# Performance work log

Measured on AMD Instinct MI355X. Metric: run time of the kernel, lower is better.

The kernel has to match this reference:

```python
import jax, jax.numpy as jnp
import numpy as np
from jax.ops import segment_sum, segment_max

N_M = 100000   # muon nodes
N_J = 100000   # jet nodes
E   = 1600000  # edges per relation (~avg degree 16)
D   = 64       # input feature dim
H   = 64       # hidden_channels
C   = 2        # num_classes

def setup_inputs():
    key = jax.random.key(0)
    ks = jax.random.split(key, 16)
    g = lambda k, shape, fan: jax.random.normal(k, shape, jnp.float32) / np.sqrt(fan).astype(np.float32)
    return {
        "x_muons": jax.random.normal(ks[0], (N_M, D), jnp.float32),
        "x_jets":  jax.random.normal(ks[1], (N_J, D), jnp.float32),
        "ei_mm": jax.random.randint(ks[2], (2, E), 0, N_M, jnp.int32),
        "ei_mj": jnp.stack([jax.random.randint(ks[3], (E,), 0, N_M, jnp.int32),
                            jax.random.randint(ks[4], (E,), 0, N_J, jnp.int32)]),
        "ei_jj": jax.random.randint(ks[5], (2, E), 0, N_J, jnp.int32),
        "gat_w_src": g(ks[6], (D, H), D),
        "gat_w_dst": g(ks[7], (D, H), D),
        "gat_att_src": g(ks[8], (H,), H),
        "gat_att_dst": g(ks[9], (H,), H),
        "gat_bias": jnp.zeros((H,), jnp.float32),
        "sage_w_l": g(ks[10], (D, H), D),
        "sage_w_r": g(ks[11], (D, H), D),
        "sage_bias": jnp.zeros((H,), jnp.float32),
        "gcn_w": g(ks[12], (D, H), D),
        "gcn_bias": jnp.zeros((H,), jnp.float32),
        "lin_w": g(ks[13], (H, C), H),
        "lin_b": jnp.zeros((C,), jnp.float32),
    }

def _add_self_loops(ei, n):
    loop = jnp.arange(n, dtype=ei.dtype)
    return jnp.concatenate([ei[0], loop]), jnp.concatenate([ei[1], loop])

def _gat(x, ei, w_src, w_dst, att_src, att_dst, bias):
    # PyG GATConv, heads=1, add_self_loops=True, negative_slope=0.2
    n = x.shape[0]
    src, dst = _add_self_loops(ei, n)
    hs = x @ w_src                      # [n, H] source-side messages
    hd = x @ w_dst                      # dst-side (attention only)
    a = jax.nn.leaky_relu((hs @ att_src)[src] + (hd @ att_dst)[dst], 0.2)
    m = segment_max(a, dst, num_segments=n)      # per-dst softmax (stable)
    ea = jnp.exp(a - m[dst])
    z = segment_sum(ea, dst, num_segments=n)
    alpha = ea / z[dst]                 # self loop guarantees z > 0
    return segment_sum(alpha[:, None] * hs[src], dst, num_segments=n) + bias

def _sage(x_src, x_dst, ei, w_l, w_r, bias):
    # PyG SAGEConv: mean aggregation, root weight, no self loops
    n = x_dst.shape[0]
    src, dst = ei[0], ei[1]
    agg = segment_sum(x_src[src], dst, num_segments=n)
    cnt = segment_sum(jnp.ones_like(dst, jnp.float32), dst, num_segments=n)
    mean = agg / jnp.maximum(cnt, 1.0)[:, None]
    return mean @ w_l + x_dst @ w_r + bias

def _gcn(x, ei, w, bias):
    # PyG GCNConv: symmetric gcn_norm on A + I
    n = x.shape[0]
    src, dst = _add_self_loops(ei, n)
    xw = x @ w
    deg = segment_sum(jnp.ones_like(dst, jnp.float32), dst, num_segments=n)
    dis = deg ** -0.5                   # deg >= 1 due to self loops
    norm = dis[src] * dis[dst]
    return segment_sum(norm[:, None] * xw[src], dst, num_segments=n) + bias

def reference(x_muons, x_jets, ei_mm, ei_mj, ei_jj,
              gat_w_src, gat_w_dst, gat_att_src, gat_att_dst, gat_bias,
              sage_w_l, sage_w_r, sage_bias, gcn_w, gcn_bias, lin_w, lin_b):
    # Original forward returns inside the layer loop -> exactly one HeteroConv layer runs.
    muons = _gat(x_muons, ei_mm, gat_w_src, gat_w_dst, gat_att_src, gat_att_dst, gat_bias)
    jets = (_sage(x_muons, x_jets, ei_mj, sage_w_l, sage_w_r, sage_bias)
            + _gcn(x_jets, ei_jj, gcn_w, gcn_bias))   # HeteroConv aggr='sum' on dst type 'jets'
    muons = jax.nn.relu(muons)
    jets = jax.nn.relu(jets)
    out = jnp.concatenate([muons, jets], axis=0)       # [N_M + N_J, H]
    return jax.nn.sigmoid(out @ lin_w + lin_b)
```

## Files before the change

kernel.cpp:

```cpp
#include <hip/hip_runtime.h>
#include <math.h>

#define N_M 100000
#define N_J 100000
#define NE  1600000
#define NTOT (3*N_M)
#define ETOT (3*NE)
#define NB_SCAN 293
#define DD  64
#define HH  64

#define NBIN 586
#define BIN_SHIFT 9
#define G1 640
#define EPB ((ETOT + G1 - 1) / G1)

__device__ __forceinline__ float lrelu(float a){ return a > 0.f ? a : 0.2f*a; }
__device__ __forceinline__ float wmax(float v){
    #pragma unroll
    for (int o = 32; o; o >>= 1) v = fmaxf(v, __shfl_xor(v, o));
    return v;
}
__device__ __forceinline__ float wsum(float v){
    #pragma unroll
    for (int o = 32; o; o >>= 1) v += __shfl_xor(v, o);
    return v;
}
__device__ __forceinline__ float sigm(float x){ return 1.f/(1.f + expf(-x)); }

__device__ __forceinline__ unsigned short f2bf(float f){
    unsigned u = __float_as_uint(f);
    u += 0x7FFFu + ((u >> 16) & 1u);
    return (unsigned short)(u >> 16);
}
__device__ __forceinline__ float bf2f(unsigned short h){
    return __uint_as_float((unsigned)h << 16);
}


__global__ void k_vdst(const float* __restrict__ w_dst, const float* __restrict__ att_dst,
                       float* __restrict__ v_dst){
    int d = threadIdx.x;
    float s = 0.f;
    for (int h = 0; h < HH; ++h) s += w_dst[d*HH + h] * att_dst[h];
    v_dst[d] = s;
}

__global__ __launch_bounds__(256) void k_muon_prep(
    const float* __restrict__ x, const float* __restrict__ w_src,
    const float* __restrict__ att_src, const float* __restrict__ v_dst,
    unsigned short* __restrict__ hs_b, float* __restrict__ as_, float* __restrict__ ad_)
{
    __shared__ float lw[DD*HH];
    __shared__ float latt[HH];
    __shared__ float lvd[DD];
    int tid = threadIdx.x;
    for (int i = tid; i < DD*HH; i += 256) lw[i] = w_src[i];
    if (tid < HH) latt[tid] = att_src[tid];
    if (tid < DD) lvd[tid] = v_dst[tid];
    __syncthreads();
    int row = blockIdx.x*64 + (tid >> 2);
    int q = tid & 3;
    if (row >= N_M) return;
    const float4* x4 = (const float4*)(x + (size_t)row*DD);
    float acc[16];
    #pragma unroll
    for (int f = 0; f < 16; ++f) acc[f] = 0.f;
    float adp = 0.f;
    for (int kk = 0; kk < 16; ++kk){
        float4 xv = x4[kk];
        adp += xv.x*lvd[4*kk] + xv.y*lvd[4*kk+1] + xv.z*lvd[4*kk+2] + xv.w*lvd[4*kk+3];
        float xs[4] = {xv.x, xv.y, xv.z, xv.w};
        #pragma unroll
        for (int j = 0; j < 4; ++j){
            const float* wp = lw + (4*kk + j)*HH + (q << 4);
            float xk = xs[j];
            #pragma unroll
            for (int f = 0; f < 16; ++f) acc[f] = fmaf(xk, wp[f], acc[f]);
        }
    }
    float asp = 0.f;
    #pragma unroll
    for (int f = 0; f < 16; ++f) asp += acc[f] * latt[(q<<4) + f];
    asp += __shfl_xor(asp, 1);
    asp += __shfl_xor(asp, 2);
    unsigned short* hp = hs_b + (size_t)row*HH + (q << 4);
    #pragma unroll
    for (int j = 0; j < 4; ++j)
        ((ushort4*)hp)[j] = make_ushort4(f2bf(acc[4*j]), f2bf(acc[4*j+1]),
                                         f2bf(acc[4*j+2]), f2bf(acc[4*j+3]));
    if (q == 0){ as_[row] = asp; ad_[row] = adp; }
}

__global__ __launch_bounds__(256) void k_gcn_xw(
    const float* __restrict__ x, const float* __restrict__ w, unsigned short* __restrict__ xw_b)
{
    __shared__ float lw[DD*HH];
    int tid = threadIdx.x;
    for (int i = tid; i < DD*HH; i += 256) lw[i] = w[i];
    __syncthreads();
    int row = blockIdx.x*64 + (tid >> 2);
    int q = tid & 3;
    if (row >= N_J) return;
    const float4* x4 = (const float4*)(x + (size_t)row*DD);
    float acc[16];
    #pragma unroll
    for (int f = 0; f < 16; ++f) acc[f] = 0.f;
    for (int kk = 0; kk < 16; ++kk){
        float4 xv = x4[kk];
        float xs[4] = {xv.x, xv.y, xv.z, xv.w};
        #pragma unroll
        for (int j = 0; j < 4; ++j){
            const float* wp = lw + (4*kk + j)*HH + (q << 4);
            float xk = xs[j];
            #pragma unroll
            for (int f = 0; f < 16; ++f) acc[f] = fmaf(xk, wp[f], acc[f]);
        }
    }
    unsigned short* hp = xw_b + (size_t)row*HH + (q << 4);
    #pragma unroll
    for (int j = 0; j < 4; ++j)
        ((ushort4*)hp)[j] = make_ushort4(f2bf(acc[4*j]), f2bf(acc[4*j+1]),
                                         f2bf(acc[4*j+2]), f2bf(acc[4*j+3]));
}

__global__ __launch_bounds__(256) void k_xr(
    const float* __restrict__ x, const float* __restrict__ w_r,
    const float* __restrict__ sb, const float* __restrict__ gb, float* __restrict__ xr)
{
    __shared__ float lw[DD*HH];
    __shared__ float lb[HH];
    int tid = threadIdx.x;
    for (int i = tid; i < DD*HH; i += 256) lw[i] = w_r[i];
    if (tid < HH) lb[tid] = sb[tid] + gb[tid];
    __syncthreads();
    int row = blockIdx.x*64 + (tid >> 2);
    int q = tid & 3;
    if (row >= N_J) return;
    const float4* x4 = (const float4*)(x + (size_t)row*DD);
    float acc[16];
    #pragma unroll
    for (int f = 0; f < 16; ++f) acc[f] = 0.f;
    for (int kk = 0; kk < 16; ++kk){
        float4 xv = x4[kk];
        float xs[4] = {xv.x, xv.y, xv.z, xv.w};
        #pragma unroll
        for (int j = 0; j < 4; ++j){
            const float* wp = lw + (4*kk + j)*HH + (q << 4);
            float xk = xs[j];
            #pragma unroll
            for (int f = 0; f < 16; ++f) acc[f] = fmaf(xk, wp[f], acc[f]);
        }
    }
    float* hp = xr + (size_t)row*HH + (q << 4);
    #pragma unroll
    for (int j = 0; j < 4; ++j){
        int f0 = (q << 4) + 4*j;
        ((float4*)hp)[j] = make_float4(acc[4*j]   + lb[f0],
                                       acc[4*j+1] + lb[f0+1],
                                       acc[4*j+2] + lb[f0+2],
                                       acc[4*j+3] + lb[f0+3]);
    }
}

__global__ void k_xm(const float* __restrict__ x, unsigned short* __restrict__ xb){
    int i = blockIdx.x*256 + threadIdx.x;
    if (i >= N_M*DD/4) return;
    float4 v = ((const float4*)x)[i];
    ((ushort4*)xb)[i] = make_ushort4(f2bf(v.x), f2bf(v.y), f2bf(v.z), f2bf(v.w));
}


__device__ __forceinline__ void edge_rd(int t, const int* ei_mm, const int* ei_mj,
                                        const int* ei_jj, const int** ei, int* r, int* e){
    if (t < NE){ *r = 0; *e = t; *ei = ei_mm; }
    else if (t < 2*NE){ *r = 1; *e = t - NE; *ei = ei_mj; }
    else { *r = 2; *e = t - 2*NE; *ei = ei_jj; }
}

__global__ __launch_bounds__(256) void k_bin0(
    const int* __restrict__ ei_mm, const int* __restrict__ ei_mj,
    const int* __restrict__ ei_jj, int* __restrict__ g_bincnt)
{
    __shared__ int bh[NBIN];
    int tid = threadIdx.x;
    for (int i = tid; i < NBIN; i += 256) bh[i] = 0;
    __syncthreads();
    int t0 = blockIdx.x * EPB;
    int t1 = min(t0 + EPB, ETOT);
    for (int t = t0 + tid; t < t1; t += 256){
        const int* ei; int r, e;
        edge_rd(t, ei_mm, ei_mj, ei_jj, &ei, &r, &e);
        int bucket = r*N_M + ei[NE + e];
        atomicAdd(&bh[bucket >> BIN_SHIFT], 1);
    }
    __syncthreads();
    for (int i = tid; i < NBIN; i += 256)
        if (bh[i]) atomicAdd(&g_bincnt[i], bh[i]);
}

__global__ void k_binscan(const int* __restrict__ g_bincnt, int* __restrict__ g_binoff,
                          int* __restrict__ g_bincur, int* __restrict__ offs)
{
    int l = threadIdx.x;
    int base = l * 10;
    int v[10]; int s = 0;
    #pragma unroll
    for (int k = 0; k < 10; ++k){
        int idx = base + k;
        v[k] = (idx < NBIN) ? g_bincnt[idx] : 0;
        s += v[k];
    }
    int inc = s;
    #pragma unroll
    for (int o = 1; o < 64; o <<= 1){
        int u = __shfl_up(inc, o);
        if (l >= o) inc += u;
    }
    int ex = inc - s;
    #pragma unroll
    for (int k = 0; k < 10; ++k){
        int idx = base + k;
        if (idx < NBIN){ g_binoff[idx] = ex; g_bincur[idx] = ex; ex += v[k]; }
    }
    if (l == 63) g_binoff[NBIN] = ex;
    if (l == 0)  offs[NTOT] = ETOT;
}

__global__ __launch_bounds__(256) void k_bin1(
    const int* __restrict__ ei_mm, const int* __restrict__ ei_mj,
    const int* __restrict__ ei_jj, int* __restrict__ g_bincur,
    unsigned* __restrict__ binned)
{
    __shared__ int bh[NBIN];
    __shared__ int cb[NBIN];
    int tid = threadIdx.x;
    for (int i = tid; i < NBIN; i += 256) bh[i] = 0;
    __syncthreads();
    int t0 = blockIdx.x * EPB;
    int t1 = min(t0 + EPB, ETOT);
    for (int t = t0 + tid; t < t1; t += 256){
        const int* ei; int r, e;
        edge_rd(t, ei_mm, ei_mj, ei_jj, &ei, &r, &e);
        int bucket = r*N_M + ei[NE + e];
        atomicAdd(&bh[bucket >> BIN_SHIFT], 1);
    }
    __syncthreads();
    for (int i = tid; i < NBIN; i += 256){
        int c = bh[i];
        cb[i] = c ? atomicAdd(&g_bincur[i], c) : 0;
        bh[i] = 0;
    }
    __syncthreads();
    for (int t = t0 + tid; t < t1; t += 256){
        const int* ei; int r, e;
        edge_rd(t, ei_mm, ei_mj, ei_jj, &ei, &r, &e);
        int s = ei[e];
        int bucket = r*N_M + ei[NE + e];
        int bin = bucket >> BIN_SHIFT;
        int lb  = bucket & 511;
        int pos = cb[bin] + atomicAdd(&bh[bin], 1);
        binned[pos] = ((unsigned)lb << 17) | (unsigned)s;
    }
}

__global__ __launch_bounds__(256) void k_build(
    const unsigned* __restrict__ binned, const int* __restrict__ g_binoff,
    int* __restrict__ offs, int* __restrict__ perm)
{
    __shared__ int lh[512];
    __shared__ int lcur[512];
    __shared__ int ls[256];
    int b = blockIdx.x, tid = threadIdx.x;
    int e0 = g_binoff[b], e1 = g_binoff[b+1];
    lh[tid] = 0; lh[tid + 256] = 0;
    __syncthreads();
    for (int e = e0 + tid; e < e1; e += 256)
        atomicAdd(&lh[binned[e] >> 17], 1);
    __syncthreads();
    int a0 = lh[2*tid], a1 = lh[2*tid + 1];
    int s = a0 + a1;
    ls[tid] = s; __syncthreads();
    for (int o = 1; o < 256; o <<= 1){
        int u = (tid >= o) ? ls[tid - o] : 0;
        __syncthreads();
        ls[tid] += u;
        __syncthreads();
    }
    int ex = ls[tid] - s;
    lcur[2*tid]     = ex;
    lcur[2*tid + 1] = ex + a0;
    int gb = b*512 + 2*tid;
    if (gb     < NTOT) offs[gb]     = e0 + ex;
    if (gb + 1 < NTOT) offs[gb + 1] = e0 + ex + a0;
    __syncthreads();
    for (int e = e0 + tid; e < e1; e += 256){
        unsigned p = binned[e];
        int pos = atomicAdd(&lcur[p >> 17], 1);
        perm[e0 + pos] = (int)(p & 0x1FFFFu);
    }
}


__global__ void k_hist(const int* __restrict__ ei_mm, const int* __restrict__ ei_mj,
                       const int* __restrict__ ei_jj, int* __restrict__ cnt){
    int t = blockIdx.x*256 + threadIdx.x;
    if (t >= ETOT) return;
    const int* ei; int r, e;
    edge_rd(t, ei_mm, ei_mj, ei_jj, &ei, &r, &e);
    atomicAdd(&cnt[r*N_M + ei[NE + e]], 1);
}

__global__ __launch_bounds__(256) void k_scan1(const int* __restrict__ cnt,
                                               int* __restrict__ offs, int* __restrict__ bsum){
    __shared__ int ls[256];
    int b = blockIdx.x, t = threadIdx.x;
    int base = b*1024 + t*4;
    int4 c = make_int4(0,0,0,0);
    if (base < NTOT) c = *(const int4*)(cnt + base);
    int s = c.x + c.y + c.z + c.w;
    ls[t] = s; __syncthreads();
    for (int o = 1; o < 256; o <<= 1){
        int a = (t >= o) ? ls[t - o] : 0;
        __syncthreads();
        ls[t] += a;
        __syncthreads();
    }
    int excl = ls[t] - s;
    if (t == 255) bsum[b] = ls[255];
    if (base < NTOT){
        offs[base]   = excl;
        offs[base+1] = excl + c.x;
        offs[base+2] = excl + c.x + c.y;
        offs[base+3] = excl + c.x + c.y + c.z;
    }
}

__global__ __launch_bounds__(512) void k_scan2(int* __restrict__ bsum){
    __shared__ int ls[512];
    int t = threadIdx.x;
    int v = (t < NB_SCAN) ? bsum[t] : 0;
    ls[t] = v; __syncthreads();
    for (int o = 1; o < 512; o <<= 1){
        int a = (t >= o) ? ls[t - o] : 0;
        __syncthreads();
        ls[t] += a;
        __syncthreads();
    }
    if (t < NB_SCAN) bsum[t] = ls[t] - v;
}

__global__ void k_scan3(int* __restrict__ offs, const int* __restrict__ bsum){
    int b = blockIdx.x, t = threadIdx.x;
    int base = b*1024 + t*4;
    if (base >= NTOT) return;
    int add = bsum[b];
    int4* p = (int4*)(offs + base);
    int4 v = *p;
    v.x += add; v.y += add; v.z += add; v.w += add;
    *p = v;
}

__global__ void k_fill(const int* __restrict__ ei_mm, const int* __restrict__ ei_mj,
                       const int* __restrict__ ei_jj, const int* __restrict__ offs,
                       int* __restrict__ cursor, int* __restrict__ perm){
    int t = blockIdx.x*256 + threadIdx.x;
    if (t >= ETOT) return;
    const int* ei; int r, e;
    edge_rd(t, ei_mm, ei_mj, ei_jj, &ei, &r, &e);
    int s = ei[e];
    int bkt = r*N_M + ei[NE + e];
    int pos = atomicAdd(&cursor[bkt], 1);
    perm[offs[bkt] + pos] = s;
}

__global__ void k_set_offs_top(int* __restrict__ offs){ offs[NTOT] = ETOT; }

__global__ void k_dis(const int* __restrict__ offs, float* __restrict__ dis){
    int j = blockIdx.x*256 + threadIdx.x;
    if (j >= N_J) return;
    int beg = offs[2*N_M + j];
    int end = (j == N_J-1) ? ETOT : offs[2*N_M + j + 1];
    dis[j] = rsqrtf((float)(end - beg + 1));
}


__global__ __launch_bounds__(512) void k_muon_gat_out(
    const int* __restrict__ offs, const int* __restrict__ perm,
    const float* __restrict__ as_, const float* __restrict__ ad_,
    const unsigned short* __restrict__ hs_b, const float* __restrict__ gat_bias,
    const float* __restrict__ lin_w, const float* __restrict__ lin_b,
    float* __restrict__ out)
{
    int wid = threadIdx.x >> 6;
    int l = threadIdx.x & 63;
    int d = blockIdx.x*8 + wid;
    if (d >= N_M) return;
    int p = l & 15, g = l >> 4;
    int beg = offs[d], end = offs[d+1];
    float ad_d = ad_[d];
    float a_self = lrelu(as_[d] + ad_d);
    float am = a_self;
    for (int base = beg; base < end; base += 64){
        int e = base + l;
        if (e < end) am = fmaxf(am, lrelu(as_[perm[e]] + ad_d));
    }
    float m = wmax(am);
    float eself = expf(a_self - m);
    float z = eself;
    float acc0 = 0.f, acc1 = 0.f, acc2 = 0.f, acc3 = 0.f;
    for (int base = beg; base < end; base += 64){
        int e = base + l;
        int sB = 0; float eaB = 0.f;
        if (e < end){
            sB = perm[e];
            eaB = expf(lrelu(as_[sB] + ad_d) - m);
        }
        z += wsum(eaB);
        int cc = min(64, end - base);
        int k = 0;
        for (; k + 16 <= cc; k += 16){
            #pragma unroll
            for (int qq = 0; qq < 4; ++qq){
                int idx = k + qq*4 + g;
                int s = __shfl(sB, idx);
                float w = __shfl(eaB, idx);
                ushort4 v = *(const ushort4*)(hs_b + (size_t)s*HH + 4*p);
                acc0 = fmaf(w, bf2f(v.x), acc0);
                acc1 = fmaf(w, bf2f(v.y), acc1);
                acc2 = fmaf(w, bf2f(v.z), acc2);
                acc3 = fmaf(w, bf2f(v.w), acc3);
            }
        }
        for (; k < cc; k += 4){
            int idx = k + g;
            int cl = min(idx, cc - 1);
            int s = __shfl(sB, cl);
            float w = __shfl(eaB, cl);
            if (idx >= cc) w = 0.f;
            ushort4 v = *(const ushort4*)(hs_b + (size_t)s*HH + 4*p);
            acc0 = fmaf(w, bf2f(v.x), acc0);
            acc1 = fmaf(w, bf2f(v.y), acc1);
            acc2 = fmaf(w, bf2f(v.z), acc2);
            acc3 = fmaf(w, bf2f(v.w), acc3);
        }
    }
    acc0 += __shfl_xor(acc0, 16); acc0 += __shfl_xor(acc0, 32);
    acc1 += __shfl_xor(acc1, 16); acc1 += __shfl_xor(acc1, 32);
    acc2 += __shfl_xor(acc2, 16); acc2 += __shfl_xor(acc2, 32);
    acc3 += __shfl_xor(acc3, 16); acc3 += __shfl_xor(acc3, 32);
    ushort4 hv = *(const ushort4*)(hs_b + (size_t)d*HH + 4*p);
    acc0 = fmaf(eself, bf2f(hv.x), acc0);
    acc1 = fmaf(eself, bf2f(hv.y), acc1);
    acc2 = fmaf(eself, bf2f(hv.z), acc2);
    acc3 = fmaf(eself, bf2f(hv.w), acc3);
    float rz = 1.f / z;
    float q0 = 0.f, q1 = 0.f;
    {
        float a[4] = {acc0, acc1, acc2, acc3};
        #pragma unroll
        for (int c = 0; c < 4; ++c){
            int f = 4*p + c;
            float val = fmaxf(a[c]*rz + gat_bias[f], 0.f);
            q0 = fmaf(val, lin_w[f*2 + 0], q0);
            q1 = fmaf(val, lin_w[f*2 + 1], q1);
        }
    }
    #pragma unroll
    for (int o = 1; o <= 8; o <<= 1){ q0 += __shfl_xor(q0, o); q1 += __shfl_xor(q1, o); }
    if (l == 0){
        size_t oo = (size_t)d*2;
        out[oo]   = sigm(q0 + lin_b[0]);
        out[oo+1] = sigm(q1 + lin_b[1]);
    }
}

__global__ __launch_bounds__(512) void k_jet_out(
    const unsigned short* __restrict__ xm_b, const unsigned short* __restrict__ xw_b,
    const float* __restrict__ xr, const float* __restrict__ dis,
    const int* __restrict__ offs, const int* __restrict__ perm,
    const float* __restrict__ w_l,
    const float* __restrict__ lin_w, const float* __restrict__ lin_b,
    float* __restrict__ out)
{
    __shared__ float lwl[DD*HH];
    int tid = threadIdx.x;
    for (int i = tid; i < DD*HH; i += 512) lwl[i] = w_l[i];
    __syncthreads();
    int wid = tid >> 6;
    int l = tid & 63;
    int j = blockIdx.x*8 + wid;
    if (j >= N_J) return;
    int p = l & 15, g = l >> 4;
    int beg = offs[N_M + j], end = offs[N_M + j + 1];
    float sa0 = 0.f, sa1 = 0.f, sa2 = 0.f, sa3 = 0.f;
    for (int base = beg; base < end; base += 64){
        int e = base + l;
        int sB = (e < end) ? perm[e] : 0;
        int cc = min(64, end - base);
        int k = 0;
        for (; k + 16 <= cc; k += 16){
            #pragma unroll
            for (int qq = 0; qq < 4; ++qq){
                int idx = k + qq*4 + g;
                int s = __shfl(sB, idx);
                ushort4 v = *(const ushort4*)(xm_b + (size_t)s*DD + 4*p);
                sa0 += bf2f(v.x); sa1 += bf2f(v.y); sa2 += bf2f(v.z); sa3 += bf2f(v.w);
            }
        }
        for (; k < cc; k += 4){
            int idx = k + g;
            int cl = min(idx, cc - 1);
            int s = __shfl(sB, cl);
            float w = (idx < cc) ? 1.f : 0.f;
            ushort4 v = *(const ushort4*)(xm_b + (size_t)s*DD + 4*p);
            sa0 = fmaf(w, bf2f(v.x), sa0);
            sa1 = fmaf(w, bf2f(v.y), sa1);
            sa2 = fmaf(w, bf2f(v.z), sa2);
            sa3 = fmaf(w, bf2f(v.w), sa3);
        }
    }
    sa0 += __shfl_xor(sa0, 16); sa0 += __shfl_xor(sa0, 32);
    sa1 += __shfl_xor(sa1, 16); sa1 += __shfl_xor(sa1, 32);
    sa2 += __shfl_xor(sa2, 16); sa2 += __shfl_xor(sa2, 32);
    sa3 += __shfl_xor(sa3, 16); sa3 += __shfl_xor(sa3, 32);
    float inv = (end > beg) ? 1.f/(float)(end - beg) : 1.f;
    float mean_a[4] = {sa0*inv, sa1*inv, sa2*inv, sa3*inv};
    int beg2 = offs[2*N_M + j];
    int end2 = (j == N_J-1) ? ETOT : offs[2*N_M + j + 1];
    float dj = dis[j];
    float gc0 = 0.f, gc1 = 0.f, gc2 = 0.f, gc3 = 0.f;
    for (int base = beg2; base < end2; base += 64){
        int e = base + l;
        int sB = 0; float nB = 0.f;
        if (e < end2){ sB = perm[e]; nB = dis[sB]*dj; }
        int cc = min(64, end2 - base);
        int k = 0;
        for (; k + 16 <= cc; k += 16){
            #pragma unroll
            for (int qq = 0; qq < 4; ++qq){
                int idx = k + qq*4 + g;
                int s = __shfl(sB, idx);
                float w = __shfl(nB, idx);
                ushort4 v = *(const ushort4*)(xw_b + (size_t)s*HH + 4*p);
                gc0 = fmaf(w, bf2f(v.x), gc0);
                gc1 = fmaf(w, bf2f(v.y), gc1);
                gc2 = fmaf(w, bf2f(v.z), gc2);
                gc3 = fmaf(w, bf2f(v.w), gc3);
            }
        }
        for (; k < cc; k += 4){
            int idx = k + g;
            int cl = min(idx, cc - 1);
            int s = __shfl(sB, cl);
            float w = __shfl(nB, cl);
            if (idx >= cc) w = 0.f;
            ushort4 v = *(const ushort4*)(xw_b + (size_t)s*HH + 4*p);
            gc0 = fmaf(w, bf2f(v.x), gc0);
            gc1 = fmaf(w, bf2f(v.y), gc1);
            gc2 = fmaf(w, bf2f(v.z), gc2);
            gc3 = fmaf(w, bf2f(v.w), gc3);
        }
    }
    gc0 += __shfl_xor(gc0, 16); gc0 += __shfl_xor(gc0, 32);
    gc1 += __shfl_xor(gc1, 16); gc1 += __shfl_xor(gc1, 32);
    gc2 += __shfl_xor(gc2, 16); gc2 += __shfl_xor(gc2, 32);
    gc3 += __shfl_xor(gc3, 16); gc3 += __shfl_xor(gc3, 32);
    {
        ushort4 sv = *(const ushort4*)(xw_b + (size_t)j*HH + 4*p);
        float djj = dj*dj;
        gc0 = fmaf(djj, bf2f(sv.x), gc0);
        gc1 = fmaf(djj, bf2f(sv.y), gc1);
        gc2 = fmaf(djj, bf2f(sv.z), gc2);
        gc3 = fmaf(djj, bf2f(sv.w), gc3);
    }
    float b0 = __shfl(gc0, l >> 2), b1 = __shfl(gc1, l >> 2);
    float b2 = __shfl(gc2, l >> 2), b3 = __shfl(gc3, l >> 2);
    int c2 = l & 3;
    float accg_lin = (c2 == 0) ? b0 : ((c2 == 1) ? b1 : ((c2 == 2) ? b2 : b3));
    float xacc = 0.f;
    #pragma unroll
    for (int k = 0; k < 64; ++k){
        float mk = __shfl(mean_a[k & 3], k >> 2);
        xacc = fmaf(mk, lwl[k*64 + l], xacc);
    }
    float val = fmaxf(xacc + accg_lin + xr[(size_t)j*HH + l], 0.f);
    float q0 = wsum(val * lin_w[l*2 + 0]);
    float q1 = wsum(val * lin_w[l*2 + 1]);
    if (l == 0){
        size_t oo = (size_t)(N_M + j)*2;
        out[oo]   = sigm(q0 + lin_b[0]);
        out[oo+1] = sigm(q1 + lin_b[1]);
    }
}

extern "C" void kernel_launch(void* const* d_in, const int* in_sizes, int n_in,
                              void* d_out, int out_size, void* d_ws, size_t ws_size,
                              hipStream_t stream) {
    const float* x_muons   = (const float*)d_in[0];
    const float* x_jets    = (const float*)d_in[1];
    const int*   ei_mm     = (const int*)d_in[2];
    const int*   ei_mj     = (const int*)d_in[3];
    const int*   ei_jj     = (const int*)d_in[4];
    const float* gat_w_src = (const float*)d_in[5];
    const float* gat_w_dst = (const float*)d_in[6];
    const float* gat_att_s = (const float*)d_in[7];
    const float* gat_att_d = (const float*)d_in[8];
    const float* gat_bias  = (const float*)d_in[9];
    const float* sage_w_l  = (const float*)d_in[10];
    const float* sage_w_r  = (const float*)d_in[11];
    const float* sage_bias = (const float*)d_in[12];
    const float* gcn_w     = (const float*)d_in[13];
    const float* gcn_bias  = (const float*)d_in[14];
    const float* lin_w     = (const float*)d_in[15];
    const float* lin_b     = (const float*)d_in[16];
    float* out = (float*)d_out;

    float* ws = (float*)d_ws;
    size_t o = 0;
    unsigned short* hs_b = (unsigned short*)(ws + o); o += (size_t)N_M*HH/2;
    unsigned short* xw_b = (unsigned short*)(ws + o); o += (size_t)N_J*HH/2;
    unsigned short* xm_b = (unsigned short*)(ws + o); o += (size_t)N_M*DD/2;
    float* xr    = ws + o; o += (size_t)N_J*HH;
    float* as_   = ws + o; o += N_M;
    float* ad_   = ws + o; o += N_M;
    float* dis   = ws + o; o += N_J;
    float* v_dst = ws + o; o += 64;
    int* offs   = (int*)(ws + o); o += NTOT + 4;
    int* perm   = (int*)(ws + o); o += ETOT;
    size_t o_common = o;

    int nb64_m = (N_M + 63) / 64;
    int nb64_j = (N_J + 63) / 64;

    k_vdst<<<1, 64, 0, stream>>>(gat_w_dst, gat_att_d, v_dst);
    k_muon_prep<<<nb64_m, 256, 0, stream>>>(x_muons, gat_w_src, gat_att_s, v_dst, hs_b, as_, ad_);
    k_gcn_xw<<<nb64_j, 256, 0, stream>>>(x_jets, gcn_w, xw_b);
    k_xr<<<nb64_j, 256, 0, stream>>>(x_jets, sage_w_r, sage_bias, gcn_bias, xr);
    k_xm<<<(N_M*DD/4 + 255)/256, 256, 0, stream>>>(x_muons, xm_b);

    size_t need_fast = (o_common + ETOT + 3*NBIN + 16) * sizeof(float);
    if (ws_size >= need_fast){
        unsigned* binned = (unsigned*)(ws + o); o += ETOT;
        int* g_bincnt    = (int*)(ws + o); o += NBIN;
        int* g_binoff    = (int*)(ws + o); o += NBIN + 4;
        int* g_bincur    = (int*)(ws + o); o += NBIN;
        hipMemsetAsync(g_bincnt, 0, NBIN*sizeof(int), stream);
        k_bin0<<<G1, 256, 0, stream>>>(ei_mm, ei_mj, ei_jj, g_bincnt);
        k_binscan<<<1, 64, 0, stream>>>(g_bincnt, g_binoff, g_bincur, offs);
        k_bin1<<<G1, 256, 0, stream>>>(ei_mm, ei_mj, ei_jj, g_bincur, binned);
        k_build<<<NBIN, 256, 0, stream>>>(binned, g_binoff, offs, perm);
    } else {
        int* cnt    = (int*)(ws + o); o += NTOT;
        int* cursor = (int*)(ws + o); o += NTOT;
        int* bsum   = (int*)(ws + o); o += 512;
        hipMemsetAsync(cnt,    0, (size_t)NTOT*sizeof(int), stream);
        hipMemsetAsync(cursor, 0, (size_t)NTOT*sizeof(int), stream);
        int nbE3 = (ETOT + 255) / 256;
        k_hist<<<nbE3, 256, 0, stream>>>(ei_mm, ei_mj, ei_jj, cnt);
        k_scan1<<<NB_SCAN, 256, 0, stream>>>(cnt, offs, bsum);
        k_scan2<<<1, 512, 0, stream>>>(bsum);
        k_scan3<<<NB_SCAN, 256, 0, stream>>>(offs, bsum);
        k_fill<<<nbE3, 256, 0, stream>>>(ei_mm, ei_mj, ei_jj, offs, cursor, perm);
        k_set_offs_top<<<1, 1, 0, stream>>>(offs);
    }

    k_dis<<<(N_J + 255)/256, 256, 0, stream>>>(offs, dis);

    k_muon_gat_out<<<(N_M + 7)/8, 512, 0, stream>>>(offs, perm, as_, ad_, hs_b,
                                                    gat_bias, lin_w, lin_b, out);
    k_jet_out<<<(N_J + 7)/8, 512, 0, stream>>>(xm_b, xw_b, xr, dis, offs, perm,
                                               sage_w_l, lin_w, lin_b, out);
}
```

Before: 422.0 us.

## Fuse bf16 cast into muon prep, online softmax, pre-gather edge scalars, merge jet loops

```diff
diff --git a/kernel.cpp b/kernel.cpp
--- a/kernel.cpp
+++ b/kernel.cpp
@@ -15,7 +15,7 @@
 #define G1 640
 #define EPB ((ETOT + G1 - 1) / G1)
 
-__device__ __forceinline__ float lrelu(float a){ return a > 0.f ? a : 0.2f*a; }
+__device__ __forceinline__ float lrelu(float a){ return fmaxf(a, 0.2f*a); }
 __device__ __forceinline__ float wmax(float v){
     #pragma unroll
     for (int o = 32; o; o >>= 1) v = fmaxf(v, __shfl_xor(v, o));
@@ -49,7 +49,8 @@
 __global__ __launch_bounds__(256) void k_muon_prep(
     const float* __restrict__ x, const float* __restrict__ w_src,
     const float* __restrict__ att_src, const float* __restrict__ v_dst,
-    unsigned short* __restrict__ hs_b, float* __restrict__ as_, float* __restrict__ ad_)
+    unsigned short* __restrict__ hs_b, float* __restrict__ as_, float* __restrict__ ad_,
+    unsigned short* __restrict__ xm_b)
 {
     __shared__ float lw[DD*HH];
     __shared__ float latt[HH];
@@ -70,6 +71,9 @@
     for (int kk = 0; kk < 16; ++kk){
         float4 xv = x4[kk];
         adp += xv.x*lvd[4*kk] + xv.y*lvd[4*kk+1] + xv.z*lvd[4*kk+2] + xv.w*lvd[4*kk+3];
+        if ((kk >> 2) == q)
+            *(ushort4*)(xm_b + (size_t)row*DD + 4*kk) =
+                make_ushort4(f2bf(xv.x), f2bf(xv.y), f2bf(xv.z), f2bf(xv.w));
         float xs[4] = {xv.x, xv.y, xv.z, xv.w};
         #pragma unroll
         for (int j = 0; j < 4; ++j){
@@ -161,13 +165,6 @@
                                        acc[4*j+2] + lb[f0+2],
                                        acc[4*j+3] + lb[f0+3]);
     }
-}
-
-__global__ void k_xm(const float* __restrict__ x, unsigned short* __restrict__ xb){
-    int i = blockIdx.x*256 + threadIdx.x;
-    if (i >= N_M*DD/4) return;
-    float4 v = ((const float4*)x)[i];
-    ((ushort4*)xb)[i] = make_ushort4(f2bf(v.x), f2bf(v.y), f2bf(v.z), f2bf(v.w));
 }
 
 
@@ -384,9 +381,17 @@
     dis[j] = rsqrtf((float)(end - beg + 1));
 }
 
+__global__ void k_val(const int* __restrict__ perm, const float* __restrict__ as_,
+                      const float* __restrict__ dis, float* __restrict__ val){
+    int t = blockIdx.x*256 + threadIdx.x;
+    if (t < NE)            val[t] = as_[perm[t]];
+    else if (t >= 2*NE && t < ETOT) val[t] = dis[perm[t]];
+}
+
 
 __global__ __launch_bounds__(512) void k_muon_gat_out(
     const int* __restrict__ offs, const int* __restrict__ perm,
+    const float* __restrict__ val,
     const float* __restrict__ as_, const float* __restrict__ ad_,
     const unsigned short* __restrict__ hs_b, const float* __restrict__ gat_bias,
     const float* __restrict__ lin_w, const float* __restrict__ lin_b,
@@ -400,28 +405,25 @@
     int beg = offs[d], end = offs[d+1];
     float ad_d = ad_[d];
     float a_self = lrelu(as_[d] + ad_d);
-    float am = a_self;
-    for (int base = beg; base < end; base += 64){
-        int e = base + l;
-        if (e < end) am = fmaxf(am, lrelu(as_[perm[e]] + ad_d));
-    }
-    float m = wmax(am);
-    float eself = expf(a_self - m);
-    float z = eself;
+    float m = a_self, z = 0.f;
     float acc0 = 0.f, acc1 = 0.f, acc2 = 0.f, acc3 = 0.f;
     for (int base = beg; base < end; base += 64){
         int e = base + l;
-        int sB = 0; float eaB = 0.f;
-        if (e < end){
-            sB = perm[e];
-            eaB = expf(lrelu(as_[sB] + ad_d) - m);
-        }
+        int sB = 0; float aB = -1e30f;
+        if (e < end){ sB = perm[e]; aB = lrelu(val[e] + ad_d); }
+        float bm = wmax(aB);
+        if (bm > m){
+            float sc = expf(m - bm);
+            acc0 *= sc; acc1 *= sc; acc2 *= sc; acc3 *= sc; z *= sc;
+            m = bm;
+        }
+        float eaB = expf(aB - m);
         z += wsum(eaB);
         int cc = min(64, end - base);
         int k = 0;
-        for (; k + 16 <= cc; k += 16){
+        for (; k + 32 <= cc; k += 32){
             #pragma unroll
-            for (int qq = 0; qq < 4; ++qq){
+            for (int qq = 0; qq < 8; ++qq){
                 int idx = k + qq*4 + g;
                 int s = __shfl(sB, idx);
                 float w = __shfl(eaB, idx);
@@ -449,6 +451,8 @@
     acc1 += __shfl_xor(acc1, 16); acc1 += __shfl_xor(acc1, 32);
     acc2 += __shfl_xor(acc2, 16); acc2 += __shfl_xor(acc2, 32);
     acc3 += __shfl_xor(acc3, 16); acc3 += __shfl_xor(acc3, 32);
+    float eself = expf(a_self - m);
+    z += eself;
     ushort4 hv = *(const ushort4*)(hs_b + (size_t)d*HH + 4*p);
     acc0 = fmaf(eself, bf2f(hv.x), acc0);
     acc1 = fmaf(eself, bf2f(hv.y), acc1);
@@ -461,9 +465,9 @@
         #pragma unroll
         for (int c = 0; c < 4; ++c){
             int f = 4*p + c;
-            float val = fmaxf(a[c]*rz + gat_bias[f], 0.f);
-            q0 = fmaf(val, lin_w[f*2 + 0], q0);
-            q1 = fmaf(val, lin_w[f*2 + 1], q1);
+            float v2 = fmaxf(a[c]*rz + gat_bias[f], 0.f);
+            q0 = fmaf(v2, lin_w[f*2 + 0], q0);
+            q1 = fmaf(v2, lin_w[f*2 + 1], q1);
         }
     }
     #pragma unroll
@@ -479,7 +483,7 @@
     const unsigned short* __restrict__ xm_b, const unsigned short* __restrict__ xw_b,
     const float* __restrict__ xr, const float* __restrict__ dis,
     const int* __restrict__ offs, const int* __restrict__ perm,
-    const float* __restrict__ w_l,
+    const float* __restrict__ val, const float* __restrict__ w_l,
     const float* __restrict__ lin_w, const float* __restrict__ lin_b,
     float* __restrict__ out)
 {
@@ -492,56 +496,64 @@
     int j = blockIdx.x*8 + wid;
     if (j >= N_J) return;
     int p = l & 15, g = l >> 4;
-    int beg = offs[N_M + j], end = offs[N_M + j + 1];
-    float sa0 = 0.f, sa1 = 0.f, sa2 = 0.f, sa3 = 0.f;
-    for (int base = beg; base < end; base += 64){
-        int e = base + l;
-        int sB = (e < end) ? perm[e] : 0;
-        int cc = min(64, end - base);
-        int k = 0;
-        for (; k + 16 <= cc; k += 16){
-            #pragma unroll
-            for (int qq = 0; qq < 4; ++qq){
-                int idx = k + qq*4 + g;
-                int s = __shfl(sB, idx);
-                ushort4 v = *(const ushort4*)(xm_b + (size_t)s*DD + 4*p);
-                sa0 += bf2f(v.x); sa1 += bf2f(v.y); sa2 += bf2f(v.z); sa3 += bf2f(v.w);
-            }
-        }
-        for (; k < cc; k += 4){
-            int idx = k + g;
-            int cl = min(idx, cc - 1);
-            int s = __shfl(sB, cl);
-            float w = (idx < cc) ? 1.f : 0.f;
-            ushort4 v = *(const ushort4*)(xm_b + (size_t)s*DD + 4*p);
-            sa0 = fmaf(w, bf2f(v.x), sa0);
-            sa1 = fmaf(w, bf2f(v.y), sa1);
-            sa2 = fmaf(w, bf2f(v.z), sa2);
-            sa3 = fmaf(w, bf2f(v.w), sa3);
-        }
-    }
-    sa0 += __shfl_xor(sa0, 16); sa0 += __shfl_xor(sa0, 32);
-    sa1 += __shfl_xor(sa1, 16); sa1 += __shfl_xor(sa1, 32);
-    sa2 += __shfl_xor(sa2, 16); sa2 += __shfl_xor(sa2, 32);
-    sa3 += __shfl_xor(sa3, 16); sa3 += __shfl_xor(sa3, 32);
-    float inv = (end > beg) ? 1.f/(float)(end - beg) : 1.f;
-    float mean_a[4] = {sa0*inv, sa1*inv, sa2*inv, sa3*inv};
+    int beg1 = offs[N_M + j],  end1 = offs[N_M + j + 1];
     int beg2 = offs[2*N_M + j];
     int end2 = (j == N_J-1) ? ETOT : offs[2*N_M + j + 1];
     float dj = dis[j];
+    float sa0 = 0.f, sa1 = 0.f, sa2 = 0.f, sa3 = 0.f;
     float gc0 = 0.f, gc1 = 0.f, gc2 = 0.f, gc3 = 0.f;
-    for (int base = beg2; base < end2; base += 64){
-        int e = base + l;
-        int sB = 0; float nB = 0.f;
-        if (e < end2){ sB = perm[e]; nB = dis[sB]*dj; }
-        int cc = min(64, end2 - base);
-        int k = 0;
-        for (; k + 16 <= cc; k += 16){
-            #pragma unroll
-            for (int qq = 0; qq < 4; ++qq){
-                int idx = k + qq*4 + g;
-                int s = __shfl(sB, idx);
-                float w = __shfl(nB, idx);
+    for (int b1 = beg1, b2 = beg2; b1 < end1 || b2 < end2; b1 += 64, b2 += 64){
+        int e1 = b1 + l, e2 = b2 + l;
+        bool h1 = (b1 < end1), h2 = (b2 < end2);
+        int sB1 = 0, sB2 = 0; float nB2 = 0.f;
+        if (h1 && e1 < end1) sB1 = perm[e1];
+        if (h2 && e2 < end2){ sB2 = perm[e2]; nB2 = val[e2]*dj; }
+        if (h1){
+            int cc = min(64, end1 - b1);
+            int k = 0;
+            for (; k + 16 <= cc; k += 16){
+                #pragma unroll
+                for (int qq = 0; qq < 4; ++qq){
+                    int idx = k + qq*4 + g;
+                    int s = __shfl(sB1, idx);
+                    ushort4 v = *(const ushort4*)(xm_b + (size_t)s*DD + 4*p);
+                    sa0 += bf2f(v.x); sa1 += bf2f(v.y); sa2 += bf2f(v.z); sa3 += bf2f(v.w);
+                }
+            }
+            for (; k < cc; k += 4){
+                int idx = k + g;
+                int cl = min(idx, cc - 1);
+                int s = __shfl(sB1, cl);
+                float w = (idx < cc) ? 1.f : 0.f;
+                ushort4 v = *(const ushort4*)(xm_b + (size_t)s*DD + 4*p);
+                sa0 = fmaf(w, bf2f(v.x), sa0);
+                sa1 = fmaf(w, bf2f(v.y), sa1);
+                sa2 = fmaf(w, bf2f(v.z), sa2);
+                sa3 = fmaf(w, bf2f(v.w), sa3);
+            }
+        }
+        if (h2){
+            int cc = min(64, end2 - b2);
+            int k = 0;
+            for (; k + 16 <= cc; k += 16){
+                #pragma unroll
+                for (int qq = 0; qq < 4; ++qq){
+                    int idx = k + qq*4 + g;
+                    int s = __shfl(sB2, idx);
+                    float w = __shfl(nB2, idx);
+                    ushort4 v = *(const ushort4*)(xw_b + (size_t)s*HH + 4*p);
+                    gc0 = fmaf(w, bf2f(v.x), gc0);
+                    gc1 = fmaf(w, bf2f(v.y), gc1);
+                    gc2 = fmaf(w, bf2f(v.z), gc2);
+                    gc3 = fmaf(w, bf2f(v.w), gc3);
+                }
+            }
+            for (; k < cc; k += 4){
+                int idx = k + g;
+                int cl = min(idx, cc - 1);
+                int s = __shfl(sB2, cl);
+                float w = __shfl(nB2, cl);
+                if (idx >= cc) w = 0.f;
                 ushort4 v = *(const ushort4*)(xw_b + (size_t)s*HH + 4*p);
                 gc0 = fmaf(w, bf2f(v.x), gc0);
                 gc1 = fmaf(w, bf2f(v.y), gc1);
@@ -549,23 +561,17 @@
                 gc3 = fmaf(w, bf2f(v.w), gc3);
             }
         }
-        for (; k < cc; k += 4){
-            int idx = k + g;
-            int cl = min(idx, cc - 1);
-            int s = __shfl(sB, cl);
-            float w = __shfl(nB, cl);
-            if (idx >= cc) w = 0.f;
-            ushort4 v = *(const ushort4*)(xw_b + (size_t)s*HH + 4*p);
-            gc0 = fmaf(w, bf2f(v.x), gc0);
-            gc1 = fmaf(w, bf2f(v.y), gc1);
-            gc2 = fmaf(w, bf2f(v.z), gc2);
-            gc3 = fmaf(w, bf2f(v.w), gc3);
-        }
-    }
+    }
+    sa0 += __shfl_xor(sa0, 16); sa0 += __shfl_xor(sa0, 32);
+    sa1 += __shfl_xor(sa1, 16); sa1 += __shfl_xor(sa1, 32);
+    sa2 += __shfl_xor(sa2, 16); sa2 += __shfl_xor(sa2, 32);
+    sa3 += __shfl_xor(sa3, 16); sa3 += __shfl_xor(sa3, 32);
     gc0 += __shfl_xor(gc0, 16); gc0 += __shfl_xor(gc0, 32);
     gc1 += __shfl_xor(gc1, 16); gc1 += __shfl_xor(gc1, 32);
     gc2 += __shfl_xor(gc2, 16); gc2 += __shfl_xor(gc2, 32);
     gc3 += __shfl_xor(gc3, 16); gc3 += __shfl_xor(gc3, 32);
+    float inv = (end1 > beg1) ? 1.f/(float)(end1 - beg1) : 1.f;
+    float mean_a[4] = {sa0*inv, sa1*inv, sa2*inv, sa3*inv};
     {
         ushort4 sv = *(const ushort4*)(xw_b + (size_t)j*HH + 4*p);
         float djj = dj*dj;
@@ -584,9 +590,9 @@
         float mk = __shfl(mean_a[k & 3], k >> 2);
         xacc = fmaf(mk, lwl[k*64 + l], xacc);
     }
-    float val = fmaxf(xacc + accg_lin + xr[(size_t)j*HH + l], 0.f);
-    float q0 = wsum(val * lin_w[l*2 + 0]);
-    float q1 = wsum(val * lin_w[l*2 + 1]);
+    float v2 = fmaxf(xacc + accg_lin + xr[(size_t)j*HH + l], 0.f);
+    float q0 = wsum(v2 * lin_w[l*2 + 0]);
+    float q1 = wsum(v2 * lin_w[l*2 + 1]);
     if (l == 0){
         size_t oo = (size_t)(N_M + j)*2;
         out[oo]   = sigm(q0 + lin_b[0]);
@@ -634,17 +640,19 @@
     int nb64_j = (N_J + 63) / 64;
 
     k_vdst<<<1, 64, 0, stream>>>(gat_w_dst, gat_att_d, v_dst);
-    k_muon_prep<<<nb64_m, 256, 0, stream>>>(x_muons, gat_w_src, gat_att_s, v_dst, hs_b, as_, ad_);
+    k_muon_prep<<<nb64_m, 256, 0, stream>>>(x_muons, gat_w_src, gat_att_s, v_dst,
+                                            hs_b, as_, ad_, xm_b);
     k_gcn_xw<<<nb64_j, 256, 0, stream>>>(x_jets, gcn_w, xw_b);
     k_xr<<<nb64_j, 256, 0, stream>>>(x_jets, sage_w_r, sage_bias, gcn_bias, xr);
-    k_xm<<<(N_M*DD/4 + 255)/256, 256, 0, stream>>>(x_muons, xm_b);
-
+
+    float* val;
     size_t need_fast = (o_common + ETOT + 3*NBIN + 16) * sizeof(float);
     if (ws_size >= need_fast){
         unsigned* binned = (unsigned*)(ws + o); o += ETOT;
         int* g_bincnt    = (int*)(ws + o); o += NBIN;
         int* g_binoff    = (int*)(ws + o); o += NBIN + 4;
         int* g_bincur    = (int*)(ws + o); o += NBIN;
+        val = (float*)binned;
         hipMemsetAsync(g_bincnt, 0, NBIN*sizeof(int), stream);
         k_bin0<<<G1, 256, 0, stream>>>(ei_mm, ei_mj, ei_jj, g_bincnt);
         k_binscan<<<1, 64, 0, stream>>>(g_bincnt, g_binoff, g_bincur, offs);
@@ -654,6 +662,7 @@
         int* cnt    = (int*)(ws + o); o += NTOT;
         int* cursor = (int*)(ws + o); o += NTOT;
         int* bsum   = (int*)(ws + o); o += 512;
+        val = ws + o; o += ETOT;
         hipMemsetAsync(cnt,    0, (size_t)NTOT*sizeof(int), stream);
         hipMemsetAsync(cursor, 0, (size_t)NTOT*sizeof(int), stream);
         int nbE3 = (ETOT + 255) / 256;
@@ -666,9 +675,10 @@
     }
 
     k_dis<<<(N_J + 255)/256, 256, 0, stream>>>(offs, dis);
-
-    k_muon_gat_out<<<(N_M + 7)/8, 512, 0, stream>>>(offs, perm, as_, ad_, hs_b,
+    k_val<<<(ETOT + 255)/256, 256, 0, stream>>>(perm, as_, dis, val);
+
+    k_muon_gat_out<<<(N_M + 7)/8, 512, 0, stream>>>(offs, perm, val, as_, ad_, hs_b,
                                                     gat_bias, lin_w, lin_b, out);
-    k_jet_out<<<(N_J + 7)/8, 512, 0, stream>>>(xm_b, xw_b, xr, dis, offs, perm,
+    k_jet_out<<<(N_J + 7)/8, 512, 0, stream>>>(xm_b, xw_b, xr, dis, offs, perm, val,
                                                sage_w_l, lin_w, lin_b, out);
 }
```

Result: slower. 441.3 us (+4.6%).
